# Performance work log

Hardware: AMD Instinct MI355X
Metric: run time of the kernel (lower is better)

Reference implementation:

```python
import jax, jax.numpy as jnp
import numpy as np

B, H = 4096, 1024
N1, N2, N3 = 28, 280, 2800  # nodes (== classes == paths) per level, branching [28,10,10]


def setup_inputs() -> dict:
    key = jax.random.key(0)
    ks = jax.random.split(key, 8)
    s = 1.0 / np.sqrt(H)  # torch nn.Linear default init bound
    x = jax.random.normal(ks[0], (B, H), jnp.float32)
    labels = jax.random.randint(ks[1], (B,), 0, N3, dtype=jnp.int32)
    W1 = jax.random.uniform(ks[2], (N1, H), jnp.float32, -s, s)
    b1 = jax.random.uniform(ks[3], (N1,), jnp.float32, -s, s)
    W2 = jax.random.uniform(ks[4], (N2, H), jnp.float32, -s, s)
    b2 = jax.random.uniform(ks[5], (N2,), jnp.float32, -s, s)
    W3 = jax.random.uniform(ks[6], (N3, H), jnp.float32, -s, s)
    b3 = jax.random.uniform(ks[7], (N3,), jnp.float32, -s, s)
    return {"x": x, "labels": labels, "W1": W1, "b1": b1,
            "W2": W2, "b2": b2, "W3": W3, "b3": b3}


def _ce(logits, lab):
    # mean cross-entropy, same as torch.nn.CrossEntropyLoss (mean reduction)
    lp = jax.nn.log_softmax(logits, axis=-1)
    return -jnp.take_along_axis(lp, lab[:, None], axis=1).mean()


def reference(x, labels, W1, b1, W2, b2, W3, b3):
    # per-level node probabilities: one grouped GEMM per level replaces the
    # Python loop of tiny Linear(hidden,1)+sigmoid calls
    z1 = jax.nn.sigmoid(x @ W1.T + b1)  # [B, N1]
    z2 = jax.nn.sigmoid(x @ W2.T + b2)  # [B, N2]
    z3 = jax.nn.sigmoid(x @ W3.T + b3)  # [B, N3]

    # path (prefix) matrices: leaf k has path [k//100, k//10, k].
    # NOTE: all nodes of a path index into the CURRENT level's weights,
    # exactly as self.nodes[lvl][node] does in the source.
    i2 = jnp.arange(N2)
    p2 = jnp.stack([i2 // 10, i2], axis=1)                    # [N2, 2]
    i3 = jnp.arange(N3)
    p3 = jnp.stack([i3 // 100, i3 // 10, i3], axis=1)          # [N3, 3]

    logits1 = z1                                               # prod over length-1 path
    logits2 = jnp.prod(z2[:, p2], axis=-1)                     # [B, N2]
    logits3 = jnp.prod(z3[:, p3], axis=-1)                     # [B, N3]

    # update_label_per_lvl: label -> ancestor node id at that level
    lab1 = labels // 100
    lab2 = labels // 10
    loss = _ce(logits1, lab1) + _ce(logits2, lab2) + _ce(logits3, labels)
    return logits3, loss
```

## Files before the change

kernel.cpp:

```cpp
#include <hip/hip_runtime.h>
#include <cstdint>


typedef unsigned short u16;
typedef unsigned char u8;
typedef long i64;
typedef float f32x4 __attribute__((ext_vector_type(4)));

#define AS_G __attribute__((address_space(1)))
#define AS_L __attribute__((address_space(3)))

constexpr int BATCH = 4096;
constexpr int H     = 1024;
constexpr int N1 = 28, N2 = 280, N3 = 2800;
constexpr int NT = N1 + N2 + N3;
constexpr int NP = 3200;
constexpr int NANC = N1 + N2 + 280;
constexpr float WSCALE = 16.0f;
constexpr float WINV   = 1.0f / 16.0f;

__device__ inline u16 f2bf(float f) {
    unsigned int u = __float_as_uint(f);
    u += 0x7fffu + ((u >> 16) & 1u);
    return (u16)(u >> 16);
}
__device__ inline float bf2f(unsigned int u) { return __uint_as_float(u << 16); }

__device__ inline unsigned int pk4_fp8(float a, float b, float c, float d) {
    unsigned int r = __builtin_amdgcn_cvt_pk_fp8_f32(a, b, 0, false);
    r = __builtin_amdgcn_cvt_pk_fp8_f32(c, d, (int)r, true);
    return r;
}

constexpr int XG = (BATCH * H) / 4;
constexpr int WG = (NP * H) / 4;
constexpr int BG = NP / 4;

__global__ __launch_bounds__(256) void cast_kernel(
        const float* __restrict__ x,
        const float* __restrict__ W1, const float* __restrict__ W2,
        const float* __restrict__ W3,
        const float* __restrict__ b1, const float* __restrict__ b2,
        const float* __restrict__ b3,
        u8* __restrict__ Xq, u8* __restrict__ Wq, float* __restrict__ biasf) {
    int g = blockIdx.x * 256 + threadIdx.x;
    if (g < XG) {
        float4 v = ((const float4*)x)[g];
        ((unsigned int*)Xq)[g] = pk4_fp8(v.x, v.y, v.z, v.w);
    } else if (g < XG + WG) {
        int wg = g - XG;
        int row = wg >> 8, cg = wg & 255;
        float4 v = make_float4(0.f, 0.f, 0.f, 0.f);
        if (row < N1)           v = ((const float4*)W1)[row * 256 + cg];
        else if (row < N1 + N2) v = ((const float4*)W2)[(row - N1) * 256 + cg];
        else if (row < NT)      v = ((const float4*)W3)[(row - N1 - N2) * 256 + cg];
        ((unsigned int*)Wq)[wg] = pk4_fp8(v.x * WSCALE, v.y * WSCALE, v.z * WSCALE, v.w * WSCALE);
    } else if (g < XG + WG + BG) {
        int bg = g - XG - WG;
        float4 v; float* vp = &v.x;
        #pragma unroll
        for (int i = 0; i < 4; ++i) {
            int c = bg * 4 + i; float t = 0.f;
            if (c < N1)           t = b1[c];
            else if (c < N1 + N2) t = b2[c - N1];
            else if (c < NT)      t = b3[c - N1 - N2];
            vp[i] = t;
        }
        ((float4*)biasf)[bg] = v;
    }
}

__global__ __launch_bounds__(256) void gemm_sig(
        const u8* __restrict__ Xq, const u8* __restrict__ Wq,
        const float* __restrict__ biasf, u16* __restrict__ Zb) {
    __shared__ __align__(16) u8 As[2][2 * 64 * 32];
    __shared__ __align__(16) u8 Bs[2][2 * 128 * 32];

    const int id  = blockIdx.x;
    const int xcd = id & 7;
    const int j   = id >> 3;
    const int m0 = ((xcd << 3) | (j & 7)) * 64;
    const int n0 = (j >> 3) * 128;

    const int tid  = threadIdx.x;
    const int lane = tid & 63;
    const int wave = tid >> 6;
    const int wr = wave >> 1;
    const int wc = wave & 1;

    const int laneM = lane & 15;
    const int u   = lane >> 4;
    const int xb  = (laneM >> 2) & 1;
    const int laneKb = (((u >> 1) ^ xb) << 4) + (u & 1) * 8;

    const int ac = tid;
    const int apanel = ac >> 7, arem = ac & 127;
    const int arowi = arem >> 1, av = arem & 1;
    const int agoff = apanel * 32 + ((av ^ ((arowi >> 2) & 1)) << 4);
    int brow[2], bgoff[2];
    #pragma unroll
    for (int t = 0; t < 2; ++t) {
        const int c = tid + 256 * t;
        const int panel = c >> 8, rem = c & 255;
        const int row = rem >> 1, v = rem & 1;
        brow[t]  = row;
        bgoff[t] = panel * 32 + ((v ^ ((row >> 2) & 1)) << 4);
    }

    auto STAGE = [&](int bufi, int kt) {
        const int k0 = kt * 64;
        __builtin_amdgcn_global_load_lds(
            (const AS_G uint32_t*)(Xq + (size_t)(m0 + arowi) * H + k0 + agoff),
            (AS_L uint32_t*)&As[bufi][ac * 16], 16, 0, 0);
        #pragma unroll
        for (int t = 0; t < 2; ++t) {
            const int c = tid + 256 * t;
            __builtin_amdgcn_global_load_lds(
                (const AS_G uint32_t*)(Wq + (size_t)(n0 + brow[t]) * H + k0 + bgoff[t]),
                (AS_L uint32_t*)&Bs[bufi][c * 16], 16, 0, 0);
        }
    };

    f32x4 acc[2][4] = {};

    STAGE(0, 0);
    int buf = 0;
    for (int kt = 0; kt < H / 64; ++kt) {
        if (kt + 1 < H / 64) {
            STAGE(buf ^ 1, kt + 1);
            asm volatile("s_waitcnt vmcnt(3)" ::: "memory");
        } else {
            asm volatile("s_waitcnt vmcnt(0)" ::: "memory");
        }
        __builtin_amdgcn_s_barrier();
        __builtin_amdgcn_sched_barrier(0);

        #pragma unroll
        for (int p = 0; p < 2; ++p) {
            i64 af[2], bfv[4];
            #pragma unroll
            for (int i = 0; i < 2; ++i)
                af[i]  = *(const i64*)&As[buf][p * 2048 + (wr * 32 + i * 16 + laneM) * 32 + laneKb];
            #pragma unroll
            for (int i = 0; i < 4; ++i)
                bfv[i] = *(const i64*)&Bs[buf][p * 4096 + (wc * 64 + i * 16 + laneM) * 32 + laneKb];
            #pragma unroll
            for (int am = 0; am < 2; ++am)
                #pragma unroll
                for (int bn = 0; bn < 4; ++bn)
                    acc[am][bn] = __builtin_amdgcn_mfma_f32_16x16x32_fp8_fp8(
                        af[am], bfv[bn], acc[am][bn], 0, 0, 0);
        }
        __builtin_amdgcn_sched_barrier(0);
        __builtin_amdgcn_s_barrier();
        buf ^= 1;
    }

    #pragma unroll
    for (int bn = 0; bn < 4; ++bn) {
        const int col = n0 + wc * 64 + bn * 16 + laneM;
        if (col >= NT) continue;
        const float bias = biasf[col];
        #pragma unroll
        for (int am = 0; am < 2; ++am) {
            const int rbase = m0 + wr * 32 + am * 16 + (lane >> 4) * 4;
            #pragma unroll
            for (int r = 0; r < 4; ++r) {
                float v = acc[am][bn][r] * WINV + bias;
                Zb[(size_t)(rbase + r) * NP + col] = f2bf(1.0f / (1.0f + __expf(-v)));
            }
        }
    }
}

__global__ __launch_bounds__(256) void logits_loss(
        const u16* __restrict__ Zb, const int* __restrict__ labels,
        float* __restrict__ out, float* __restrict__ partials) {
    __shared__ float zs[NANC];
    __shared__ float red[12];
    const int b = blockIdx.x, tid = threadIdx.x;
    const u16* Zrow = Zb + (size_t)b * NP;

    const unsigned int* Zr = (const unsigned int*)Zrow;
    for (int i = tid; i < NANC / 2; i += 256) {
        unsigned int v = Zr[i];
        zs[2 * i]     = bf2f(v & 0xffffu);
        zs[2 * i + 1] = bf2f(v >> 16);
    }
    __syncthreads();

    float se1 = 0.f, se2 = 0.f, se3 = 0.f;
    float4* outr4 = (float4*)(out + (size_t)b * N3);
    const uint2* Z3s = (const uint2*)(Zrow + N1 + N2);
    for (int q = tid; q < N3 / 4; q += 256) {
        const uint2 zv = Z3s[q];
        float z3v[4] = { bf2f(zv.x & 0xffffu), bf2f(zv.x >> 16),
                         bf2f(zv.y & 0xffffu), bf2f(zv.y >> 16) };
        const int k = q * 4;
        float4 o; float* op = &o.x;
        #pragma unroll
        for (int uu = 0; uu < 4; ++uu) {
            const int kk = k + uu;
            float lg = z3v[uu] * zs[308 + kk / 10] * zs[308 + kk / 100];
            op[uu] = lg;
            se3 += __expf(lg);
        }
        outr4[q] = o;
    }
    for (int jj = tid; jj < N2; jj += 256)
        se2 += __expf(zs[N1 + jj] * zs[N1 + jj / 10]);
    if (tid < N1)
        se1 = __expf(zs[tid]);

    #pragma unroll
    for (int off = 32; off > 0; off >>= 1) {
        se1 += __shfl_down(se1, off, 64);
        se2 += __shfl_down(se2, off, 64);
        se3 += __shfl_down(se3, off, 64);
    }
    if ((tid & 63) == 0) {
        int w = tid >> 6;
        red[w] = se3; red[4 + w] = se2; red[8 + w] = se1;
    }
    __syncthreads();
    if (tid == 0) {
        float s3 = red[0] + red[1] + red[2] + red[3];
        float s2 = red[4] + red[5] + red[6] + red[7];
        float s1 = red[8] + red[9] + red[10] + red[11];
        int lab  = labels[b];
        int lab2 = lab / 10, lab1 = lab / 100;
        float l1 = zs[lab1];
        float l2 = zs[N1 + lab2] * zs[N1 + lab2 / 10];
        float l3 = bf2f((unsigned int)Zrow[N1 + N2 + lab]) * zs[308 + lab2] * zs[308 + lab1];
        partials[b] = (logf(s1) - l1) + (logf(s2) - l2) + (logf(s3) - l3);
    }
}

__global__ __launch_bounds__(256) void final_reduce(
        const float* __restrict__ partials, float* __restrict__ out) {
    __shared__ float red[4];
    const int tid = threadIdx.x;
    float s = 0.f;
    for (int i = tid; i < BATCH; i += 256) s += partials[i];
    #pragma unroll
    for (int off = 32; off > 0; off >>= 1) s += __shfl_down(s, off, 64);
    if ((tid & 63) == 0) red[tid >> 6] = s;
    __syncthreads();
    if (tid == 0)
        out[(size_t)BATCH * N3] = (red[0] + red[1] + red[2] + red[3]) * (1.0f / BATCH);
}

extern "C" void kernel_launch(void* const* d_in, const int* in_sizes, int n_in,
                              void* d_out, int out_size, void* d_ws, size_t ws_size,
                              hipStream_t stream) {
    const float* x      = (const float*)d_in[0];
    const int*   labels = (const int*)d_in[1];
    const float* W1     = (const float*)d_in[2];
    const float* b1     = (const float*)d_in[3];
    const float* W2     = (const float*)d_in[4];
    const float* b2     = (const float*)d_in[5];
    const float* W3     = (const float*)d_in[6];
    const float* b3     = (const float*)d_in[7];
    float* out = (float*)d_out;

    char* ws = (char*)d_ws;
    u8*    Xq       = (u8*)ws;
    u8*    Wq       = (u8*)(ws + 4194304);
    u16*   Zb       = (u16*)(ws + 7471104);
    float* biasf    = (float*)(ws + 33685504);
    float* partials = (float*)(ws + 33698304);

    cast_kernel<<<(XG + WG + BG + 255) / 256, 256, 0, stream>>>(
        x, W1, W2, W3, b1, b2, b3, Xq, Wq, biasf);
    gemm_sig<<<1600, 256, 0, stream>>>(Xq, Wq, biasf, Zb);
    logits_loss<<<BATCH, 256, 0, stream>>>(Zb, labels, out, partials);
    final_reduce<<<1, 256, 0, stream>>>(partials, out);
}
```

Before: 148.7 us.

## Enlarge GEMM tile to 128x128 and fold final reduction into loss kernel

The FP8 GEMM block tile grows from 64x128 to 128x128, so each wave computes a 64x64 sub-tile with 16 MFMA accumulators, and the grid halves to 800 blocks. This raises data reuse per LDS load and cuts redundant weight traffic, at the cost of more registers and fewer blocks in flight. Separately, the final batch reduction kernel is removed. The last logits_loss block, found through an atomic ticket counter reset in the cast kernel, now sums the partials, which saves one kernel launch.

```diff
diff --git a/kernel.cpp b/kernel.cpp
--- a/kernel.cpp
+++ b/kernel.cpp
@@ -42,8 +42,10 @@
         const float* __restrict__ W3,
         const float* __restrict__ b1, const float* __restrict__ b2,
         const float* __restrict__ b3,
-        u8* __restrict__ Xq, u8* __restrict__ Wq, float* __restrict__ biasf) {
+        u8* __restrict__ Xq, u8* __restrict__ Wq, float* __restrict__ biasf,
+        unsigned* __restrict__ counter) {
     int g = blockIdx.x * 256 + threadIdx.x;
+    if (g == 0) *counter = 0u;
     if (g < XG) {
         float4 v = ((const float4*)x)[g];
         ((unsigned int*)Xq)[g] = pk4_fp8(v.x, v.y, v.z, v.w);
@@ -73,62 +75,58 @@
 __global__ __launch_bounds__(256) void gemm_sig(
         const u8* __restrict__ Xq, const u8* __restrict__ Wq,
         const float* __restrict__ biasf, u16* __restrict__ Zb) {
-    __shared__ __align__(16) u8 As[2][2 * 64 * 32];
+    __shared__ __align__(16) u8 As[2][2 * 128 * 32];
     __shared__ __align__(16) u8 Bs[2][2 * 128 * 32];
 
     const int id  = blockIdx.x;
     const int xcd = id & 7;
     const int j   = id >> 3;
-    const int m0 = ((xcd << 3) | (j & 7)) * 64;
-    const int n0 = (j >> 3) * 128;
+    const int m0 = ((xcd << 2) | (j & 3)) * 128;
+    const int n0 = (j >> 2) * 128;
 
     const int tid  = threadIdx.x;
     const int lane = tid & 63;
     const int wave = tid >> 6;
-    const int wr = wave >> 1;
-    const int wc = wave & 1;
+    const int wm = (wave >> 1) * 64;
+    const int wn = (wave & 1) * 64;
 
     const int laneM = lane & 15;
     const int u   = lane >> 4;
     const int xb  = (laneM >> 2) & 1;
     const int laneKb = (((u >> 1) ^ xb) << 4) + (u & 1) * 8;
 
-    const int ac = tid;
-    const int apanel = ac >> 7, arem = ac & 127;
-    const int arowi = arem >> 1, av = arem & 1;
-    const int agoff = apanel * 32 + ((av ^ ((arowi >> 2) & 1)) << 4);
-    int brow[2], bgoff[2];
+    int srow[2], sgoff[2];
     #pragma unroll
     for (int t = 0; t < 2; ++t) {
         const int c = tid + 256 * t;
         const int panel = c >> 8, rem = c & 255;
         const int row = rem >> 1, v = rem & 1;
-        brow[t]  = row;
-        bgoff[t] = panel * 32 + ((v ^ ((row >> 2) & 1)) << 4);
+        srow[t]  = row;
+        sgoff[t] = panel * 32 + ((v ^ ((row >> 2) & 1)) << 4);
     }
 
     auto STAGE = [&](int bufi, int kt) {
         const int k0 = kt * 64;
-        __builtin_amdgcn_global_load_lds(
-            (const AS_G uint32_t*)(Xq + (size_t)(m0 + arowi) * H + k0 + agoff),
-            (AS_L uint32_t*)&As[bufi][ac * 16], 16, 0, 0);
         #pragma unroll
         for (int t = 0; t < 2; ++t) {
             const int c = tid + 256 * t;
             __builtin_amdgcn_global_load_lds(
-                (const AS_G uint32_t*)(Wq + (size_t)(n0 + brow[t]) * H + k0 + bgoff[t]),
+                (const AS_G uint32_t*)(Xq + (size_t)(m0 + srow[t]) * H + k0 + sgoff[t]),
+                (AS_L uint32_t*)&As[bufi][c * 16], 16, 0, 0);
+            __builtin_amdgcn_global_load_lds(
+                (const AS_G uint32_t*)(Wq + (size_t)(n0 + srow[t]) * H + k0 + sgoff[t]),
                 (AS_L uint32_t*)&Bs[bufi][c * 16], 16, 0, 0);
         }
     };
 
-    f32x4 acc[2][4] = {};
+    f32x4 acc[4][4] = {};
 
     STAGE(0, 0);
     int buf = 0;
     for (int kt = 0; kt < H / 64; ++kt) {
         if (kt + 1 < H / 64) {
             STAGE(buf ^ 1, kt + 1);
-            asm volatile("s_waitcnt vmcnt(3)" ::: "memory");
+            asm volatile("s_waitcnt vmcnt(4)" ::: "memory");
         } else {
             asm volatile("s_waitcnt vmcnt(0)" ::: "memory");
         }
@@ -137,15 +135,14 @@
 
         #pragma unroll
         for (int p = 0; p < 2; ++p) {
-            i64 af[2], bfv[4];
+            i64 af[4], bfv[4];
             #pragma unroll
-            for (int i = 0; i < 2; ++i)
-                af[i]  = *(const i64*)&As[buf][p * 2048 + (wr * 32 + i * 16 + laneM) * 32 + laneKb];
+            for (int i = 0; i < 4; ++i) {
+                af[i]  = *(const i64*)&As[buf][p * 4096 + (wm + i * 16 + laneM) * 32 + laneKb];
+                bfv[i] = *(const i64*)&Bs[buf][p * 4096 + (wn + i * 16 + laneM) * 32 + laneKb];
+            }
             #pragma unroll
-            for (int i = 0; i < 4; ++i)
-                bfv[i] = *(const i64*)&Bs[buf][p * 4096 + (wc * 64 + i * 16 + laneM) * 32 + laneKb];
-            #pragma unroll
-            for (int am = 0; am < 2; ++am)
+            for (int am = 0; am < 4; ++am)
                 #pragma unroll
                 for (int bn = 0; bn < 4; ++bn)
                     acc[am][bn] = __builtin_amdgcn_mfma_f32_16x16x32_fp8_fp8(
@@ -158,12 +155,12 @@
 
     #pragma unroll
     for (int bn = 0; bn < 4; ++bn) {
-        const int col = n0 + wc * 64 + bn * 16 + laneM;
+        const int col = n0 + wn + bn * 16 + laneM;
         if (col >= NT) continue;
         const float bias = biasf[col];
         #pragma unroll
-        for (int am = 0; am < 2; ++am) {
-            const int rbase = m0 + wr * 32 + am * 16 + (lane >> 4) * 4;
+        for (int am = 0; am < 4; ++am) {
+            const int rbase = m0 + wm + am * 16 + u * 4;
             #pragma unroll
             for (int r = 0; r < 4; ++r) {
                 float v = acc[am][bn][r] * WINV + bias;
@@ -175,9 +172,11 @@
 
 __global__ __launch_bounds__(256) void logits_loss(
         const u16* __restrict__ Zb, const int* __restrict__ labels,
-        float* __restrict__ out, float* __restrict__ partials) {
+        float* __restrict__ out, float* __restrict__ partials,
+        unsigned* __restrict__ counter) {
     __shared__ float zs[NANC];
     __shared__ float red[12];
+    __shared__ unsigned ticket_s;
     const int b = blockIdx.x, tid = threadIdx.x;
     const u16* Zrow = Zb + (size_t)b * NP;
 
@@ -234,20 +233,22 @@
         float l3 = bf2f((unsigned int)Zrow[N1 + N2 + lab]) * zs[308 + lab2] * zs[308 + lab1];
         partials[b] = (logf(s1) - l1) + (logf(s2) - l2) + (logf(s3) - l3);
     }
-}
-
-__global__ __launch_bounds__(256) void final_reduce(
-        const float* __restrict__ partials, float* __restrict__ out) {
-    __shared__ float red[4];
-    const int tid = threadIdx.x;
-    float s = 0.f;
-    for (int i = tid; i < BATCH; i += 256) s += partials[i];
-    #pragma unroll
-    for (int off = 32; off > 0; off >>= 1) s += __shfl_down(s, off, 64);
-    if ((tid & 63) == 0) red[tid >> 6] = s;
+
+    __threadfence();
+    if (tid == 0) ticket_s = atomicAdd(counter, 1u);
     __syncthreads();
-    if (tid == 0)
-        out[(size_t)BATCH * N3] = (red[0] + red[1] + red[2] + red[3]) * (1.0f / BATCH);
+    if (ticket_s == BATCH - 1) {
+        __threadfence();
+        const volatile float* vp = partials;
+        float s = 0.f;
+        for (int i = tid; i < BATCH; i += 256) s += vp[i];
+        #pragma unroll
+        for (int off = 32; off > 0; off >>= 1) s += __shfl_down(s, off, 64);
+        if ((tid & 63) == 0) red[tid >> 6] = s;
+        __syncthreads();
+        if (tid == 0)
+            out[(size_t)BATCH * N3] = (red[0] + red[1] + red[2] + red[3]) * (1.0f / BATCH);
+    }
 }
 
 extern "C" void kernel_launch(void* const* d_in, const int* in_sizes, int n_in,
@@ -269,10 +270,10 @@
     u16*   Zb       = (u16*)(ws + 7471104);
     float* biasf    = (float*)(ws + 33685504);
     float* partials = (float*)(ws + 33698304);
+    unsigned* counter = (unsigned*)(ws + 33714688);
 
     cast_kernel<<<(XG + WG + BG + 255) / 256, 256, 0, stream>>>(
-        x, W1, W2, W3, b1, b2, b3, Xq, Wq, biasf);
-    gemm_sig<<<1600, 256, 0, stream>>>(Xq, Wq, biasf, Zb);
-    logits_loss<<<BATCH, 256, 0, stream>>>(Zb, labels, out, partials);
-    final_reduce<<<1, 256, 0, stream>>>(partials, out);
-}
+        x, W1, W2, W3, b1, b2, b3, Xq, Wq, biasf, counter);
+    gemm_sig<<<800, 256, 0, stream>>>(Xq, Wq, biasf, Zb);
+    logits_loss<<<BATCH, 256, 0, stream>>>(Zb, labels, out, partials, counter);
+}
```

Result: slower. 537.1 us (+261.2%).

## Give each wave private LDS staging buffers and drop block barriers in GEMM

Applied to the files above, without the earlier changes.

Each wave now stages its own 32-row A slice and 64-row B slice into a private LDS region through direct global-to-LDS loads. Because no wave reads data staged by another wave, both s_barrier calls in the K loop are removed and the vmcnt wait is adjusted to the six loads each wave issues per stage. In exchange, A rows are now fetched twice per block (once per column wave) and B rows twice (once per row wave), which raises global/L2 traffic, and LDS use grows from 24KB to 48KB, which may reduce occupancy.

```diff
diff --git a/kernel.cpp b/kernel.cpp
--- a/kernel.cpp
+++ b/kernel.cpp
@@ -73,8 +73,7 @@
 __global__ __launch_bounds__(256) void gemm_sig(
         const u8* __restrict__ Xq, const u8* __restrict__ Wq,
         const float* __restrict__ biasf, u16* __restrict__ Zb) {
-    __shared__ __align__(16) u8 As[2][2 * 64 * 32];
-    __shared__ __align__(16) u8 Bs[2][2 * 128 * 32];
+    __shared__ __align__(16) u8 lds[4][2][6144];
 
     const int id  = blockIdx.x;
     const int xcd = id & 7;
@@ -93,57 +92,55 @@
     const int xb  = (laneM >> 2) & 1;
     const int laneKb = (((u >> 1) ^ xb) << 4) + (u & 1) * 8;
 
-    const int ac = tid;
-    const int apanel = ac >> 7, arem = ac & 127;
-    const int arowi = arem >> 1, av = arem & 1;
-    const int agoff = apanel * 32 + ((av ^ ((arowi >> 2) & 1)) << 4);
-    int brow[2], bgoff[2];
-    #pragma unroll
-    for (int t = 0; t < 2; ++t) {
-        const int c = tid + 256 * t;
-        const int panel = c >> 8, rem = c & 255;
-        const int row = rem >> 1, v = rem & 1;
-        brow[t]  = row;
-        bgoff[t] = panel * 32 + ((v ^ ((row >> 2) & 1)) << 4);
-    }
-
-    auto STAGE = [&](int bufi, int kt) {
+    const int srow = lane >> 1;
+    const int sv   = lane & 1;
+    const int sgA  = (sv ^ ((srow >> 2) & 1)) << 4;
+
+    u8* wb[2] = { &lds[wave][0][0], &lds[wave][1][0] };
+    const u8* Arow0 = Xq + (size_t)(m0 + wr * 32) * H;
+    const u8* Brow0 = Wq + (size_t)(n0 + wc * 64) * H;
+
+    auto STAGE = [&](u8* base, int kt) {
         const int k0 = kt * 64;
-        __builtin_amdgcn_global_load_lds(
-            (const AS_G uint32_t*)(Xq + (size_t)(m0 + arowi) * H + k0 + agoff),
-            (AS_L uint32_t*)&As[bufi][ac * 16], 16, 0, 0);
-        #pragma unroll
-        for (int t = 0; t < 2; ++t) {
-            const int c = tid + 256 * t;
+        #pragma unroll
+        for (int q2 = 0; q2 < 2; ++q2) {
             __builtin_amdgcn_global_load_lds(
-                (const AS_G uint32_t*)(Wq + (size_t)(n0 + brow[t]) * H + k0 + bgoff[t]),
-                (AS_L uint32_t*)&Bs[bufi][c * 16], 16, 0, 0);
+                (const AS_G uint32_t*)(Arow0 + (size_t)srow * H + k0 + q2 * 32 + sgA),
+                (AS_L uint32_t*)(base + (lane + 64 * q2) * 16), 16, 0, 0);
+        }
+        #pragma unroll
+        for (int q = 0; q < 4; ++q) {
+            const int row = (lane + 64 * (q & 1)) >> 1;
+            const int goff = (q >> 1) * 32 + ((sv ^ ((row >> 2) & 1)) << 4);
+            __builtin_amdgcn_global_load_lds(
+                (const AS_G uint32_t*)(Brow0 + (size_t)row * H + k0 + goff),
+                (AS_L uint32_t*)(base + 2048 + (lane + 64 * q) * 16), 16, 0, 0);
         }
     };
 
     f32x4 acc[2][4] = {};
 
-    STAGE(0, 0);
+    STAGE(wb[0], 0);
     int buf = 0;
     for (int kt = 0; kt < H / 64; ++kt) {
         if (kt + 1 < H / 64) {
-            STAGE(buf ^ 1, kt + 1);
-            asm volatile("s_waitcnt vmcnt(3)" ::: "memory");
+            STAGE(wb[buf ^ 1], kt + 1);
+            asm volatile("s_waitcnt vmcnt(6)" ::: "memory");
         } else {
             asm volatile("s_waitcnt vmcnt(0)" ::: "memory");
         }
-        __builtin_amdgcn_s_barrier();
         __builtin_amdgcn_sched_barrier(0);
 
+        const u8* base = wb[buf];
         #pragma unroll
         for (int p = 0; p < 2; ++p) {
             i64 af[2], bfv[4];
             #pragma unroll
             for (int i = 0; i < 2; ++i)
-                af[i]  = *(const i64*)&As[buf][p * 2048 + (wr * 32 + i * 16 + laneM) * 32 + laneKb];
+                af[i]  = *(const i64*)(base + p * 1024 + (i * 16 + laneM) * 32 + laneKb);
             #pragma unroll
             for (int i = 0; i < 4; ++i)
-                bfv[i] = *(const i64*)&Bs[buf][p * 4096 + (wc * 64 + i * 16 + laneM) * 32 + laneKb];
+                bfv[i] = *(const i64*)(base + 2048 + p * 2048 + (i * 16 + laneM) * 32 + laneKb);
             #pragma unroll
             for (int am = 0; am < 2; ++am)
                 #pragma unroll
@@ -152,7 +149,6 @@
                         af[am], bfv[bn], acc[am][bn], 0, 0, 0);
         }
         __builtin_amdgcn_sched_barrier(0);
-        __builtin_amdgcn_s_barrier();
         buf ^= 1;
     }
 
@@ -163,7 +159,7 @@
         const float bias = biasf[col];
         #pragma unroll
         for (int am = 0; am < 2; ++am) {
-            const int rbase = m0 + wr * 32 + am * 16 + (lane >> 4) * 4;
+            const int rbase = m0 + wr * 32 + am * 16 + u * 4;
             #pragma unroll
             for (int r = 0; r < 4; ++r) {
                 float v = acc[am][bn][r] * WINV + bias;
```

Result: slower. 159.6 us (+7.4%).
